# Kernel optimization log

Measured on AMD Instinct MI355X. Metric: run time of the kernel, lower is better.

Reference implementation:

```python
import jax, jax.numpy as jnp
import numpy as np


def _conv(x, w, b, stride, pad):
    y = jax.lax.conv_general_dilated(
        x, w, window_strides=(stride, stride),
        padding=((pad, pad), (pad, pad)),
        dimension_numbers=('NCHW', 'OIHW', 'NCHW'))
    return y + b[None, :, None, None]


def setup_inputs() -> dict:
    key = jax.random.key(0)
    ks = jax.random.split(key, 10)
    B, C, H, W = 4, 3, 256, 256
    HID, D, K = 128, 32, 65536
    s = 0.05
    return {
        'x': jax.random.normal(ks[0], (B, C, H, W), dtype=jnp.float32),
        'w1': jax.random.normal(ks[1], (HID, C, 4, 4), dtype=jnp.float32) * s,
        'b1': jnp.zeros((HID,), dtype=jnp.float32),
        'w2': jax.random.normal(ks[2], (HID, HID, 4, 4), dtype=jnp.float32) * s,
        'b2': jnp.zeros((HID,), dtype=jnp.float32),
        'w3': jax.random.normal(ks[3], (HID, HID, 4, 4), dtype=jnp.float32) * s,
        'b3': jnp.zeros((HID,), dtype=jnp.float32),
        'w4': jax.random.normal(ks[4], (D, HID, 3, 3), dtype=jnp.float32) * s,
        'b4': jnp.zeros((D,), dtype=jnp.float32),
        'codebook': jax.random.normal(ks[5], (K, D), dtype=jnp.float32),
    }


def reference(x, w1, b1, w2, b2, w3, b3, w4, b4, codebook):
    z = jax.nn.relu(_conv(x, w1, b1, 2, 1))
    z = jax.nn.relu(_conv(z, w2, b2, 2, 1))
    z = jax.nn.relu(_conv(z, w3, b3, 2, 1))
    z = _conv(z, w4, b4, 1, 1)                 # [B, D, h, w]
    z = jnp.transpose(z, (0, 2, 3, 1))          # [B, h, w, D]
    B, h, w, D = z.shape
    zf = z.reshape(-1, D)                        # [N, D]
    # pairwise squared distances: ||z||^2 + ||e||^2 - 2 z.e
    d = (jnp.sum(zf * zf, axis=1, keepdims=True)
         + jnp.sum(codebook * codebook, axis=1)[None, :]
         - 2.0 * jnp.matmul(zf, codebook.T))    # [N, K]
    idx = jnp.argmin(d, axis=1)                  # [N]
    z_q = codebook[idx].reshape(B, h, w, D)
    return idx.reshape(B, h, w), z_q
```

## Files before the change

### kernel.cpp

```cpp
#include <hip/hip_runtime.h>
#include <cfloat>

typedef float f32x4 __attribute__((ext_vector_type(4)));
typedef _Float16 h8 __attribute__((ext_vector_type(8)));

static __device__ __forceinline__ unsigned umin_(unsigned a, unsigned b) { return a < b ? a : b; }
static __device__ __forceinline__ unsigned umax_(unsigned a, unsigned b) { return a > b ? a : b; }
static __device__ __forceinline__ unsigned med3_(unsigned a, unsigned b, unsigned c) {
    unsigned d;
    asm("v_med3_u32 %0, %1, %2, %3" : "=v"(d) : "v"(a), "v"(b), "v"(c));
    return d;
}

static __device__ __forceinline__ void gl_lds16(const h8* g, h8* s) {
    __builtin_amdgcn_global_load_lds(
        (const __attribute__((address_space(1))) unsigned int*)g,
        (__attribute__((address_space(3))) unsigned int*)s, 16, 0, 0);
}


__global__ __launch_bounds__(256)
void zero_b_k(_Float16* p0, _Float16* p1, _Float16* p2, _Float16* p3,
              _Float16* p4, _Float16* p5) {
    const int s = blockIdx.y;
    _Float16* p; int np, P;
    switch (s) {
        case 0: p = p0; np = 16; P = 66; break;
        case 1: p = p1; np = 16; P = 66; break;
        case 2: p = p2; np = 16; P = 34; break;
        case 3: p = p3; np = 16; P = 34; break;
        case 4: p = p4; np = 4;  P = 34; break;
        default: p = p5; np = 4; P = 34; break;
    }
    const int plane = blockIdx.x;
    if (plane >= np) return;
    _Float16* pl = p + (size_t)plane * P * P * 128;
    const int rowN = P * 128;
    for (int i = threadIdx.x; i < rowN; i += 256) {
        pl[i] = (_Float16)0.f;
        pl[(size_t)(P - 1) * rowN + i] = (_Float16)0.f;
        const int r = i >> 7, c = i & 127;
        pl[(size_t)r * rowN + c] = (_Float16)0.f;
        pl[(size_t)r * rowN + (P - 1) * 128 + c] = (_Float16)0.f;
    }
}

__global__ __launch_bounds__(256)
void conv1_k(const float* __restrict__ in, const float* __restrict__ w,
             const float* __restrict__ bias,
             _Float16* __restrict__ Dh, _Float16* __restrict__ Dl) {
    __shared__ float tile[3][34 * 36];
    const int tid = threadIdx.x;
    const int tx = tid & 15, ty = tid >> 4;
    const int bx = blockIdx.x & 7, by = blockIdx.x >> 3;
    const int oc0 = blockIdx.y * 8;
    const int b = blockIdx.z;
    const int ox = bx * 16 + tx, oy = by * 16 + ty;
    const int ix0 = bx * 32 - 1, iy0 = by * 32 - 1;

    for (int f = tid; f < 3 * 34 * 34; f += 256) {
        const int ic = f / 1156, r2 = f % 1156;
        const int r = r2 / 34, c = r2 % 34;
        const int iy = iy0 + r, ix = ix0 + c;
        float v = ((unsigned)iy < 256u && (unsigned)ix < 256u)
                      ? in[((size_t)(b * 3 + ic) * 256 + iy) * 256 + ix] : 0.f;
        tile[ic][r * 36 + c] = v;
    }
    __syncthreads();

    float acc[8];
#pragma unroll
    for (int j = 0; j < 8; ++j) acc[j] = 0.f;
#pragma unroll
    for (int ic = 0; ic < 3; ++ic) {
#pragma unroll
        for (int kh = 0; kh < 4; ++kh) {
            const float2* p = (const float2*)&tile[ic][(2 * ty + kh) * 36 + 2 * tx];
            const float2 r0 = p[0], r1 = p[1];
            const float tap[4] = {r0.x, r0.y, r1.x, r1.y};
#pragma unroll
            for (int kw = 0; kw < 4; ++kw)
#pragma unroll
                for (int j = 0; j < 8; ++j)
                    acc[j] = fmaf(tap[kw], w[((oc0 + j) * 3 + ic) * 16 + kh * 4 + kw], acc[j]);
        }
    }

    h8 hv, lv;
#pragma unroll
    for (int j = 0; j < 8; ++j) {
        float r = fmaxf(acc[j] + bias[oc0 + j], 0.f);
        _Float16 h = (_Float16)r;
        hv[j] = h;
        lv[j] = (_Float16)((r - (float)h) * 2048.f);
    }
    const size_t di = (((size_t)((b * 2 + (oy & 1)) * 2 + (ox & 1)) * 66 + 1 + (oy >> 1)) * 66
                       + 1 + (ox >> 1)) * 128 + oc0;
    *(h8*)(Dh + di) = hv;
    *(h8*)(Dl + di) = lv;
}

__global__ __launch_bounds__(256)
void pack3_k(const float* __restrict__ w2, const float* __restrict__ w3,
             const float* __restrict__ w4,
             h8* __restrict__ B2h, h8* __restrict__ B2l,
             h8* __restrict__ B3h, h8* __restrict__ B3l,
             h8* __restrict__ B4h, h8* __restrict__ B4l) {
    const float* w; h8 *Bh, *Bl; int T, NT, KHKW;
    switch (blockIdx.y) {
        case 0:  w = w2; Bh = B2h; Bl = B2l; T = 16; NT = 8; KHKW = 16; break;
        case 1:  w = w3; Bh = B3h; Bl = B3l; T = 16; NT = 8; KHKW = 16; break;
        default: w = w4; Bh = B4h; Bl = B4l; T = 9;  NT = 2; KHKW = 9;  break;
    }
    const int idx = blockIdx.x * 256 + threadIdx.x;
    if (idx >= T * 4 * NT * 64) return;
    const int lane = idx & 63;
    int r = idx >> 6;
    const int nt = r % NT; r /= NT;
    const int ks = r & 3;  r >>= 2;
    const int t = r;
    const int oc = nt * 16 + (lane & 15);
    const int icb = ks * 32 + (lane >> 4) * 8;
    h8 hv, lv;
#pragma unroll
    for (int j = 0; j < 8; ++j) {
        const float v = w[(size_t)(oc * 128 + icb + j) * KHKW + t];
        _Float16 h = (_Float16)v;
        hv[j] = h;
        lv[j] = (_Float16)((v - (float)h) * 2048.f);
    }
    Bh[idx] = hv;
    Bl[idx] = lv;
}

template<int WN, int MT, bool SPLIT>
__global__ __launch_bounds__(256, 1)
void gemmS2_k(const _Float16* __restrict__ Ah, const _Float16* __restrict__ Al,
              const h8* __restrict__ Bh, const h8* __restrict__ Bl,
              const float* __restrict__ bias,
              _Float16* __restrict__ Dh, _Float16* __restrict__ Dl,
              int OW, int OH, int PP, int dPP) {
    constexpr int NW_N = 8 / WN;
    constexpr int NW_M = 4 / NW_N;
    __shared__ h8 lH[2][2048];
    __shared__ h8 lL[2][2048];

    const int tid = threadIdx.x, wid = tid >> 6, l = tid & 63;
    const int nq = wid % NW_N, mi = wid / NW_N;
    const int mt0 = (blockIdx.x * NW_M + mi) * MT;
    const int mpr = OW >> 4, mpi = OH * mpr;
    const int laneA = (l & 15) * 128 + (l >> 4) * 8;

    int bm[MT], oym[MT], oxm[MT];
#pragma unroll
    for (int m = 0; m < MT; ++m) {
        const int mt = mt0 + m;
        bm[m] = mt / mpi;
        const int rem = mt % mpi;
        oym[m] = rem / mpr;
        oxm[m] = (rem % mpr) << 4;
    }

    f32x4 a1[MT][WN], am[MT][WN];
#pragma unroll
    for (int m = 0; m < MT; ++m)
#pragma unroll
        for (int s = 0; s < WN; ++s) {
            a1[m][s] = (f32x4){0.f, 0.f, 0.f, 0.f};
            am[m][s] = (f32x4){0.f, 0.f, 0.f, 0.f};
        }

    {
        const h8* sh = Bh + wid * 512 + l;
        const h8* sl = Bl + wid * 512 + l;
#pragma unroll
        for (int i = 0; i < 8; ++i) gl_lds16(sh + i * 64, &lH[0][wid * 512 + i * 64]);
#pragma unroll
        for (int i = 0; i < 8; ++i) gl_lds16(sl + i * 64, &lL[0][wid * 512 + i * 64]);
    }
    __syncthreads();

#pragma unroll 1
    for (int t = 0; t < 16; ++t) {
        const int cur = t & 1;
        const int kh = t >> 2, kw = t & 3;
        const int dy = (kh - 1) >> 1, dx = (kw - 1) >> 1;
        const int py = (kh - 1) & 1, px = (kw - 1) & 1;
        h8 avh[MT][4], avl[MT][4];
#pragma unroll
        for (int m = 0; m < MT; ++m) {
            const int pidx = (bm[m] * 2 + py) * 2 + px;
            const size_t abase = ((size_t)(pidx * PP + (oym[m] + dy + 1)) * PP
                                  + (oxm[m] + dx + 1)) * 128 + laneA;
#pragma unroll
            for (int ks = 0; ks < 4; ++ks) {
                avh[m][ks] = *(const h8*)(Ah + abase + ks * 32);
                avl[m][ks] = *(const h8*)(Al + abase + ks * 32);
            }
        }
        if (t + 1 < 16) {
            const int nxt = cur ^ 1;
            const h8* sh = Bh + (size_t)(t + 1) * 2048 + wid * 512 + l;
            const h8* sl = Bl + (size_t)(t + 1) * 2048 + wid * 512 + l;
#pragma unroll
            for (int i = 0; i < 8; ++i) gl_lds16(sh + i * 64, &lH[nxt][wid * 512 + i * 64]);
#pragma unroll
            for (int i = 0; i < 8; ++i) gl_lds16(sl + i * 64, &lL[nxt][wid * 512 + i * 64]);
        }
#pragma unroll
        for (int ks = 0; ks < 4; ++ks) {
#pragma unroll
            for (int s = 0; s < WN; ++s) {
                const h8 bvh = lH[cur][(ks * 8 + nq * WN + s) * 64 + l];
                const h8 bvl = lL[cur][(ks * 8 + nq * WN + s) * 64 + l];
#pragma unroll
                for (int m = 0; m < MT; ++m) {
                    a1[m][s] = __builtin_amdgcn_mfma_f32_16x16x32_f16(avh[m][ks], bvh, a1[m][s], 0, 0, 0);
                    am[m][s] = __builtin_amdgcn_mfma_f32_16x16x32_f16(avh[m][ks], bvl, am[m][s], 0, 0, 0);
                    am[m][s] = __builtin_amdgcn_mfma_f32_16x16x32_f16(avl[m][ks], bvh, am[m][s], 0, 0, 0);
                }
            }
        }
        __syncthreads();
    }

#pragma unroll
    for (int m = 0; m < MT; ++m) {
#pragma unroll
        for (int s = 0; s < WN; ++s) {
            const int oc = (nq * WN + s) * 16 + (l & 15);
            const float bv = bias[oc];
#pragma unroll
            for (int i = 0; i < 4; ++i) {
                const int row = (l >> 4) * 4 + i;
                float v = fmaf(am[m][s][i], 4.8828125e-4f, a1[m][s][i]);
                v = fmaxf(v + bv, 0.f);
                _Float16 h = (_Float16)v;
                _Float16 lo = (_Float16)((v - (float)h) * 2048.f);
                const int oxp = oxm[m] + row;
                const int oy = oym[m], b = bm[m];
                size_t di;
                if constexpr (SPLIT) {
                    di = (((size_t)((b * 2 + (oy & 1)) * 2 + (oxp & 1)) * dPP
                           + 1 + (oy >> 1)) * dPP + 1 + (oxp >> 1)) * 128 + oc;
                } else {
                    di = ((size_t)(b * dPP + 1 + oy) * dPP + 1 + oxp) * 128 + oc;
                }
                Dh[di] = h;
                Dl[di] = lo;
            }
        }
    }
}

template<int S, bool FIN, int WPN, int MT>
__global__ __launch_bounds__(256)
void gemm_k(const _Float16* __restrict__ Ah, const _Float16* __restrict__ Al,
            const h8* __restrict__ Bh, const h8* __restrict__ Bl,
            float* __restrict__ part, const float* __restrict__ bias,
            _Float16* __restrict__ Dh, _Float16* __restrict__ Dl,
            int OW, int OH, int PP, int NT, int TPS, int M, int N, int dPP) {
    const int tid = threadIdx.x, wid = tid >> 6, l = tid & 63;
    const int ntb = wid % WPN;
    const int mt0 = (blockIdx.x * (4 / WPN) + wid / WPN) * MT;
    const int sp = blockIdx.y;
    const int mpr = OW >> 4, mpi = OH * mpr;
    const int laneA = (l & 15) * 128 + (l >> 4) * 8;

    int bmt[MT], oymt[MT], oxmt[MT];
#pragma unroll
    for (int m = 0; m < MT; ++m) {
        const int mt = mt0 + m;
        bmt[m] = mt / mpi;
        const int rem = mt % mpi;
        oymt[m] = rem / mpr;
        oxmt[m] = (rem % mpr) << 4;
    }

    f32x4 a1[MT][2], am[MT][2];
#pragma unroll
    for (int m = 0; m < MT; ++m)
#pragma unroll
        for (int s = 0; s < 2; ++s) {
            a1[m][s] = (f32x4){0.f, 0.f, 0.f, 0.f};
            am[m][s] = (f32x4){0.f, 0.f, 0.f, 0.f};
        }

    const int t0 = sp * TPS, t1 = t0 + TPS;
#pragma unroll 2
    for (int t = t0; t < t1; ++t) {
        int dy, dx, pidx[MT];
        if constexpr (S == 2) {
            const int kh = t >> 2, kw = t & 3;
            dy = (kh - 1) >> 1; dx = (kw - 1) >> 1;
            const int py = (kh - 1) & 1, px = (kw - 1) & 1;
#pragma unroll
            for (int m = 0; m < MT; ++m) pidx[m] = (bmt[m] * 2 + py) * 2 + px;
        } else {
            dy = t / 3 - 1; dx = t % 3 - 1;
#pragma unroll
            for (int m = 0; m < MT; ++m) pidx[m] = bmt[m];
        }
        const _Float16* pAh[MT]; const _Float16* pAl[MT];
#pragma unroll
        for (int m = 0; m < MT; ++m) {
            const size_t base = ((size_t)(pidx[m] * PP + (oymt[m] + dy + 1)) * PP
                                 + (oxmt[m] + dx + 1)) * 128 + laneA;
            pAh[m] = Ah + base;
            pAl[m] = Al + base;
        }
        const size_t bbase = ((size_t)(t * 4) * NT + ntb * 2) * 64 + l;
#pragma unroll
        for (int ks = 0; ks < 4; ++ks) {
            h8 avh[MT], avl[MT];
#pragma unroll
            for (int m = 0; m < MT; ++m) {
                avh[m] = *(const h8*)(pAh[m] + ks * 32);
                avl[m] = *(const h8*)(pAl[m] + ks * 32);
            }
#pragma unroll
            for (int s = 0; s < 2; ++s) {
                const h8 bvh = Bh[bbase + (size_t)ks * NT * 64 + s * 64];
                const h8 bvl = Bl[bbase + (size_t)ks * NT * 64 + s * 64];
#pragma unroll
                for (int m = 0; m < MT; ++m) {
                    a1[m][s] = __builtin_amdgcn_mfma_f32_16x16x32_f16(avh[m], bvh, a1[m][s], 0, 0, 0);
                    am[m][s] = __builtin_amdgcn_mfma_f32_16x16x32_f16(avh[m], bvl, am[m][s], 0, 0, 0);
                    am[m][s] = __builtin_amdgcn_mfma_f32_16x16x32_f16(avl[m], bvh, am[m][s], 0, 0, 0);
                }
            }
        }
    }

#pragma unroll
    for (int m = 0; m < MT; ++m) {
        const int mt = mt0 + m;
#pragma unroll
        for (int s = 0; s < 2; ++s) {
            const int oc = ntb * 32 + s * 16 + (l & 15);
#pragma unroll
            for (int i = 0; i < 4; ++i) {
                const int row = (l >> 4) * 4 + i;
                float v = fmaf(am[m][s][i], 4.8828125e-4f, a1[m][s][i]);
                if (!FIN) {
                    part[((size_t)sp * M + mt * 16 + row) * N + oc] = v;
                } else {
                    v = fmaxf(v + bias[oc], 0.f);
                    _Float16 h = (_Float16)v;
                    _Float16 lo = (_Float16)((v - (float)h) * 2048.f);
                    const int ox = oxmt[m] + row;
                    const int oy = oymt[m], b = bmt[m];
                    const size_t di = (((size_t)((b * 2 + (oy & 1)) * 2 + (ox & 1)) * dPP
                                        + 1 + (oy >> 1)) * dPP + 1 + (ox >> 1)) * 128 + oc;
                    Dh[di] = h;
                    Dl[di] = lo;
                }
            }
        }
    }
}

__global__ __launch_bounds__(256)
void fin4_k(const float* __restrict__ part, const float* __restrict__ bias,
            float* __restrict__ zz, h8* __restrict__ zh, h8* __restrict__ zl) {
    const int t = blockIdx.x * 256 + threadIdx.x;
    const int m = t >> 2, g8 = (t & 3) * 8;
    float v[8];
#pragma unroll
    for (int j = 0; j < 8; ++j) v[j] = bias[g8 + j];
#pragma unroll
    for (int sp = 0; sp < 3; ++sp) {
        const float4* p = (const float4*)(part + ((size_t)sp * 4096 + m) * 32 + g8);
        float4 x0 = p[0], x1 = p[1];
        v[0] += x0.x; v[1] += x0.y; v[2] += x0.z; v[3] += x0.w;
        v[4] += x1.x; v[5] += x1.y; v[6] += x1.z; v[7] += x1.w;
    }
    float4* dst = (float4*)(zz + (size_t)m * 32 + g8);
    dst[0] = make_float4(v[0], v[1], v[2], v[3]);
    dst[1] = make_float4(v[4], v[5], v[6], v[7]);
    h8 hv, lv;
#pragma unroll
    for (int j = 0; j < 8; ++j) {
        const float mv = -2.f * v[j];
        _Float16 h = (_Float16)mv;
        hv[j] = h;
        lv[j] = (_Float16)(mv - (float)h);
    }
    const int idx = (m >> 4) * 64 + (m & 15) + (t & 3) * 16;
    zh[idx] = hv;
    zl[idx] = lv;
}

#define VQ_NSPLIT 64
#define VQ_KSPC   1024
#define VQ_NCHUNK 8
#define VQ_TAU_S  102.4f
#define VQ_ABS_S  524288.0f
#define VQ_QT     4

__global__ __launch_bounds__(256)
void split_cb_k(const float* __restrict__ cb, h8* __restrict__ cbh, h8* __restrict__ cbl,
                float* __restrict__ cbn2, float* __restrict__ cbn_raw,
                unsigned* __restrict__ counter) {
    const int c = blockIdx.x * 256 + threadIdx.x;
    const float4* p = (const float4*)(cb + (size_t)c * 32);
    float e[32];
    float s = 0.f;
#pragma unroll
    for (int i = 0; i < 8; ++i) {
        float4 v = p[i];
        e[i*4+0] = v.x; e[i*4+1] = v.y; e[i*4+2] = v.z; e[i*4+3] = v.w;
        s += v.x*v.x + v.y*v.y + v.z*v.z + v.w*v.w;
    }
    cbn_raw[c] = s;
    cbn2[c]    = (s + 512.0f) * 2048.0f;
    const int base = (c >> 4) * 64 + (c & 15);
#pragma unroll
    for (int g = 0; g < 4; ++g) {
        h8 hv, lv;
#pragma unroll
        for (int j = 0; j < 8; ++j) {
            float v = e[g*8 + j];
            _Float16 h = (_Float16)v;
            hv[j] = (_Float16)((float)h * 2048.0f);
            lv[j] = (_Float16)((v - (float)h) * 2048.0f);
        }
        cbh[base + g*16] = hv;
        cbl[base + g*16] = lv;
    }
    if (c == 0) *counter = 0u;
}

__global__ __launch_bounds__(256, 4)
void vq_mfma_k(const h8* __restrict__ zh, const h8* __restrict__ zl,
               const uint4* __restrict__ cbh, const uint4* __restrict__ cbl,
               const float* __restrict__ cbn2,
               unsigned* __restrict__ pb1, unsigned* __restrict__ pb2,
               unsigned* __restrict__ pcol) {
    __shared__ uint4 lH[2][512];
    __shared__ uint4 lL[2][512];
    __shared__ float lN[2][128];

    const int tid = threadIdx.x;
    const int w = tid >> 6, ln = tid & 63;
    const int split = blockIdx.y;
    const int qt0 = (blockIdx.x * 4 + w) * VQ_QT;

    h8 azh[VQ_QT], azl[VQ_QT];
#pragma unroll
    for (int qq = 0; qq < VQ_QT; ++qq) {
        azh[qq] = zh[(qt0 + qq) * 64 + ln];
        azl[qq] = zl[(qt0 + qq) * 64 + ln];
    }

    unsigned b1[VQ_QT][4], b2[VQ_QT][4];
#pragma unroll
    for (int qq = 0; qq < VQ_QT; ++qq)
#pragma unroll
        for (int i = 0; i < 4; ++i) { b1[qq][i] = 0x7F800000u; b2[qq][i] = 0x7F800000u; }

    const int fbase = split * (VQ_KSPC * 4);
    const int nbase = split * VQ_KSPC;

    {
        uint4 h0 = cbh[fbase + tid], h1 = cbh[fbase + 256 + tid];
        uint4 l0 = cbl[fbase + tid], l1 = cbl[fbase + 256 + tid];
        lH[0][tid] = h0; lH[0][tid + 256] = h1;
        lL[0][tid] = l0; lL[0][tid + 256] = l1;
        if (tid < 128) lN[0][tid] = cbn2[nbase + tid];
    }
    __syncthreads();

    for (int ci = 0; ci < VQ_NCHUNK; ++ci) {
        const int cur = ci & 1;
        const bool more = (ci + 1 < VQ_NCHUNK);
        uint4 nh0, nh1, nl0, nl1; float nn = 0.f;
        if (more) {
            const int nb = fbase + (ci + 1) * 512;
            nh0 = cbh[nb + tid]; nh1 = cbh[nb + 256 + tid];
            nl0 = cbl[nb + tid]; nl1 = cbl[nb + 256 + tid];
            if (tid < 128) nn = cbn2[nbase + (ci + 1) * 128 + tid];
        }

        const unsigned tcb = (unsigned)(ci * 8);
#pragma unroll
        for (int t = 0; t < 8; ++t) {
            const h8 bh = *reinterpret_cast<const h8*>(&lH[cur][t*64 + ln]);
            const h8 bl = *reinterpret_cast<const h8*>(&lL[cur][t*64 + ln]);
            const float nv = lN[cur][t*16 + (ln & 15)];
            f32x4 nvv = {nv, nv, nv, nv};
            const unsigned tc = tcb + t;
#pragma unroll
            for (int qq = 0; qq < VQ_QT; ++qq) {
                f32x4 acc;
                acc = __builtin_amdgcn_mfma_f32_16x16x32_f16(azh[qq], bh, nvv, 0, 0, 0);
                acc = __builtin_amdgcn_mfma_f32_16x16x32_f16(azh[qq], bl, acc, 0, 0, 0);
                acc = __builtin_amdgcn_mfma_f32_16x16x32_f16(azl[qq], bh, acc, 0, 0, 0);
#pragma unroll
                for (int i = 0; i < 4; ++i) {
                    const unsigned k0 = (__float_as_uint(acc[i]) & 0xFFFFFF00u) | tc;
                    b2[qq][i] = med3_(b1[qq][i], b2[qq][i], k0);
                    b1[qq][i] = umin_(b1[qq][i], k0);
                }
            }
        }

        if (more) {
            const int nxt = cur ^ 1;
            lH[nxt][tid] = nh0; lH[nxt][tid + 256] = nh1;
            lL[nxt][tid] = nl0; lL[nxt][tid + 256] = nl1;
            if (tid < 128) lN[nxt][tid] = nn;
        }
        __syncthreads();
    }

#pragma unroll
    for (int qq = 0; qq < VQ_QT; ++qq) {
#pragma unroll
        for (int i = 0; i < 4; ++i) {
            unsigned v1 = b1[qq][i], v2 = b2[qq][i], cv = (unsigned)(ln & 15);
#pragma unroll
            for (int m = 1; m < 16; m <<= 1) {
                unsigned o1 = __shfl_xor(v1, m, 64);
                unsigned o2 = __shfl_xor(v2, m, 64);
                unsigned oc = __shfl_xor(cv, m, 64);
                unsigned nb2 = umin_(umin_(v2, o2), umax_(v1, o1));
                if (o1 < v1) cv = oc;
                v1 = umin_(v1, o1); v2 = nb2;
            }
            if ((ln & 15) == 0) {
                const int q = (qt0 + qq) * 16 + (ln >> 4) * 4 + i;
                pb1[(size_t)q * VQ_NSPLIT + split] = v1;
                pb2[(size_t)q * VQ_NSPLIT + split] = v2;
                pcol[(size_t)q * VQ_NSPLIT + split] = cv;
            }
        }
    }
}

__global__ __launch_bounds__(256)
void combine_k(const unsigned* __restrict__ pb1, const unsigned* __restrict__ pb2,
               const unsigned* __restrict__ pcol,
               unsigned* __restrict__ coarse, unsigned* __restrict__ flags,
               unsigned* __restrict__ list, unsigned* __restrict__ counter) {
    const int q = blockIdx.x * 256 + threadIdx.x;
    unsigned B1 = 0x7F800000u, B2 = 0x7F800000u, PAY = 0u;
#pragma unroll 4
    for (int s = 0; s < VQ_NSPLIT; ++s) {
        unsigned a1 = pb1[(size_t)q * VQ_NSPLIT + s];
        unsigned a2 = pb2[(size_t)q * VQ_NSPLIT + s];
        unsigned ac = pcol[(size_t)q * VQ_NSPLIT + s];
        unsigned nb2 = umin_(umin_(B2, a2), umax_(B1, a1));
        if (a1 < B1) PAY = ((unsigned)s << 4) | ac;
        B1 = umin_(B1, a1); B2 = nb2;
    }
    const unsigned tile = B1 & 0xFFu;
    const unsigned code = (PAY >> 4) * VQ_KSPC + tile * 16 + (PAY & 15u);
    const float f1 = __uint_as_float(B1 & 0xFFFFFF00u);
    const float f2 = __uint_as_float(B2 & 0xFFFFFF00u);
    const int fl = (f2 - f1 < VQ_TAU_S) || (f1 < VQ_ABS_S);
    coarse[q] = code;
    flags[q] = (unsigned)fl;
    if (fl) { unsigned p = atomicAdd(counter, 1u); list[p] = q; }
}

__global__ __launch_bounds__(256)
void guard_k(const float* __restrict__ cb, const float* __restrict__ cbn_raw,
             const float* __restrict__ zz, const unsigned* __restrict__ list,
             const unsigned* __restrict__ counter, float2* __restrict__ gpart) {
    __shared__ float lcb[256 * 36];
    __shared__ float lnr[256];
    __shared__ float2 red[4];
    __shared__ int ns;

    const int tid = threadIdx.x;
    const int w = tid >> 6, ln = tid & 63;
    const int bx = blockIdx.x;

    const float4* cb4 = (const float4*)cb;
#pragma unroll
    for (int it = 0; it < 8; ++it) {
        const int f = tid + it * 256;
        float4 v = cb4[(size_t)bx * 2048 + f];
        const int c = f >> 3, g = f & 7;
        *(float4*)&lcb[c * 36 + g * 4] = v;
    }
    lnr[tid] = cbn_raw[bx * 256 + tid];
    if (tid == 0) ns = (int)*(volatile unsigned*)counter;
    __syncthreads();

    for (int ii = blockIdx.y; ii < ns; ii += 8) {
        const int q = (int)list[ii];
        const float4* zq = (const float4*)(zz + (size_t)q * 32);
        float m2[32];
#pragma unroll
        for (int j = 0; j < 8; ++j) {
            float4 v = zq[j];
            m2[j*4+0] = -2.f*v.x; m2[j*4+1] = -2.f*v.y; m2[j*4+2] = -2.f*v.z; m2[j*4+3] = -2.f*v.w;
        }
        float d = lnr[tid];
#pragma unroll
        for (int j = 0; j < 8; ++j) {
            float4 e = *(const float4*)&lcb[tid * 36 + j * 4];
            d = fmaf(m2[j*4+0], e.x, d);
            d = fmaf(m2[j*4+1], e.y, d);
            d = fmaf(m2[j*4+2], e.z, d);
            d = fmaf(m2[j*4+3], e.w, d);
        }
        float bv = d; int bc = tid;
#pragma unroll
        for (int m = 1; m < 64; m <<= 1) {
            float ov = __shfl_xor(bv, m, 64);
            int   oi = __shfl_xor(bc, m, 64);
            if (ov < bv || (ov == bv && oi < bc)) { bv = ov; bc = oi; }
        }
        if (ln == 0) red[w] = make_float2(bv, (float)(bx * 256 + bc));
        __syncthreads();
        if (tid == 0) {
            float2 r = red[0];
#pragma unroll
            for (int k = 1; k < 4; ++k) {
                float2 o = red[k];
                if (o.x < r.x || (o.x == r.x && o.y < r.y)) r = o;
            }
            gpart[(size_t)q * 256 + bx] = r;
        }
        __syncthreads();
    }
}

__global__ __launch_bounds__(256)
void final_k(const unsigned* __restrict__ flags, const unsigned* __restrict__ coarse,
             const float2* __restrict__ gpart, const float* __restrict__ cb,
             float* __restrict__ out_idx, float* __restrict__ out_zq) {
    const int q = blockIdx.x * 256 + threadIdx.x;
    int bi;
    if (flags[q]) {
        float2 r = gpart[(size_t)q * 256];
        for (int b = 1; b < 256; ++b) {
            float2 o = gpart[(size_t)q * 256 + b];
            if (o.x < r.x || (o.x == r.x && o.y < r.y)) r = o;
        }
        bi = (int)r.y;
    } else {
        bi = (int)coarse[q];
    }
    out_idx[q] = (float)bi;
    const float4* src = (const float4*)(cb + (size_t)bi * 32);
    float4*       dst = (float4*)(out_zq + (size_t)q * 32);
#pragma unroll
    for (int i = 0; i < 8; ++i) dst[i] = src[i];
}

extern "C" void kernel_launch(void* const* d_in, const int* in_sizes, int n_in,
                              void* d_out, int out_size, void* d_ws, size_t ws_size,
                              hipStream_t stream) {
    const float* x  = (const float*)d_in[0];
    const float* w1 = (const float*)d_in[1];
    const float* b1 = (const float*)d_in[2];
    const float* w2 = (const float*)d_in[3];
    const float* b2 = (const float*)d_in[4];
    const float* w3 = (const float*)d_in[5];
    const float* b3 = (const float*)d_in[6];
    const float* w4 = (const float*)d_in[7];
    const float* b4 = (const float*)d_in[8];
    const float* cb = (const float*)d_in[9];
    float* out = (float*)d_out;

    float* ws = (float*)d_ws;
    _Float16* y1h = (_Float16*)ws;
    _Float16* y1l = (_Float16*)(ws + 4460544);
    _Float16* y2h = (_Float16*)(ws + 8921088);
    _Float16* y2l = (_Float16*)(ws + 10104832);
    _Float16* y3h = (_Float16*)(ws + 11288576);
    _Float16* y3l = (_Float16*)(ws + 11584512);
    float* zzp = ws + 11880448;
    h8* B2h = (h8*)(ws + 12011520);
    h8* B2l = (h8*)(ws + 12142592);
    h8* B3h = (h8*)(ws + 12273664);
    h8* B3l = (h8*)(ws + 12404736);
    h8* B4h = (h8*)(ws + 12535808);
    h8* B4l = (h8*)(ws + 12554240);
    float* part = ws + 12572672;
    h8*       cbh     = (h8*)ws;
    h8*       cbl     = (h8*)(ws + 1048576);
    h8*       zh      = (h8*)(ws + 2097152);
    h8*       zl      = (h8*)(ws + 2162688);
    float*    cbn2    = ws + 2228224;
    float*    cbn_raw = ws + 2293760;
    unsigned* pb1     = (unsigned*)(ws + 2359296);
    unsigned* pb2     = (unsigned*)(ws + 2621440);
    unsigned* pcol    = (unsigned*)(ws + 2883584);
    unsigned* coarse  = (unsigned*)(ws + 3145728);
    unsigned* flags   = (unsigned*)(ws + 3149824);
    unsigned* list    = (unsigned*)(ws + 3153920);
    unsigned* counter = (unsigned*)(ws + 3158016);
    float2*   gpart   = (float2*)(ws + 3158080);

    zero_b_k<<<dim3(16, 6), 256, 0, stream>>>(y1h, y1l, y2h, y2l, y3h, y3l);
    pack3_k<<<dim3(128, 3), 256, 0, stream>>>(w2, w3, w4, B2h, B2l, B3h, B3l, B4h, B4l);
    conv1_k<<<dim3(64, 16, 4), 256, 0, stream>>>(x, w1, b1, y1h, y1l);
    gemmS2_k<4, 2, true><<<dim3(256), 256, 0, stream>>>(y1h, y1l, B2h, B2l, b2, y2h, y2l,
                                                        64, 64, 66, 34);
    gemmS2_k<2, 1, false><<<dim3(256), 256, 0, stream>>>(y2h, y2l, B3h, B3l, b3, y3h, y3l,
                                                         32, 32, 34, 34);
    gemm_k<1, false, 1, 1><<<dim3(64, 3), 256, 0, stream>>>(y3h, y3l, B4h, B4l, part, nullptr, nullptr, nullptr,
                                                            32, 32, 34, 2, 3, 4096, 32, 0);
    fin4_k<<<64, 256, 0, stream>>>(part, b4, zzp, zh, zl);

    split_cb_k<<<256, 256, 0, stream>>>(cb, cbh, cbl, cbn2, cbn_raw, counter);
    vq_mfma_k <<<dim3(16, VQ_NSPLIT), 256, 0, stream>>>(zh, zl, (const uint4*)cbh, (const uint4*)cbl,
                                                        cbn2, pb1, pb2, pcol);
    combine_k <<<16,  256, 0, stream>>>(pb1, pb2, pcol, coarse, flags, list, counter);
    guard_k   <<<dim3(256, 8), 256, 0, stream>>>(cb, cbn_raw, zzp, list, counter, gpart);
    final_k   <<<16,  256, 0, stream>>>(flags, coarse, gpart, cb, out, out + 4096);
}
```

Measured before the change: 277.5 us.

## Give each wavefront its own query in guard and final reductions

In the guard kernel each wavefront now handles a separate flagged query and scans all 256 cached codes (4 per lane). This removes the block-wide LDS reduction and the two __syncthreads per query. The final kernel now assigns one wavefront per query and reduces the 256 partials with lanes plus shuffles, instead of one thread looping serially over 256 entries. It launches 1024 blocks instead of 16, which improves memory parallelism and spreads the gather copy across lanes.

```diff
diff --git a/kernel.cpp b/kernel.cpp
--- a/kernel.cpp
+++ b/kernel.cpp
@@ -570,7 +570,6 @@
              const unsigned* __restrict__ counter, float2* __restrict__ gpart) {
     __shared__ float lcb[256 * 36];
     __shared__ float lnr[256];
-    __shared__ float2 red[4];
     __shared__ int ns;
 
     const int tid = threadIdx.x;
@@ -589,7 +588,7 @@
     if (tid == 0) ns = (int)*(volatile unsigned*)counter;
     __syncthreads();
 
-    for (int ii = blockIdx.y; ii < ns; ii += 8) {
+    for (int ii = blockIdx.y * 4 + w; ii < ns; ii += 32) {
         const int q = (int)list[ii];
         const float4* zq = (const float4*)(zz + (size_t)q * 32);
         float m2[32];
@@ -598,34 +597,28 @@
             float4 v = zq[j];
             m2[j*4+0] = -2.f*v.x; m2[j*4+1] = -2.f*v.y; m2[j*4+2] = -2.f*v.z; m2[j*4+3] = -2.f*v.w;
         }
-        float d = lnr[tid];
-#pragma unroll
-        for (int j = 0; j < 8; ++j) {
-            float4 e = *(const float4*)&lcb[tid * 36 + j * 4];
-            d = fmaf(m2[j*4+0], e.x, d);
-            d = fmaf(m2[j*4+1], e.y, d);
-            d = fmaf(m2[j*4+2], e.z, d);
-            d = fmaf(m2[j*4+3], e.w, d);
-        }
-        float bv = d; int bc = tid;
+        float bv = FLT_MAX; int bc = 0x7FFFFFFF;
+#pragma unroll
+        for (int cc = 0; cc < 4; ++cc) {
+            const int c = cc * 64 + ln;
+            float d = lnr[c];
+#pragma unroll
+            for (int j = 0; j < 8; ++j) {
+                float4 e = *(const float4*)&lcb[c * 36 + j * 4];
+                d = fmaf(m2[j*4+0], e.x, d);
+                d = fmaf(m2[j*4+1], e.y, d);
+                d = fmaf(m2[j*4+2], e.z, d);
+                d = fmaf(m2[j*4+3], e.w, d);
+            }
+            if (d < bv || (d == bv && c < bc)) { bv = d; bc = c; }
+        }
 #pragma unroll
         for (int m = 1; m < 64; m <<= 1) {
             float ov = __shfl_xor(bv, m, 64);
             int   oi = __shfl_xor(bc, m, 64);
             if (ov < bv || (ov == bv && oi < bc)) { bv = ov; bc = oi; }
         }
-        if (ln == 0) red[w] = make_float2(bv, (float)(bx * 256 + bc));
-        __syncthreads();
-        if (tid == 0) {
-            float2 r = red[0];
-#pragma unroll
-            for (int k = 1; k < 4; ++k) {
-                float2 o = red[k];
-                if (o.x < r.x || (o.x == r.x && o.y < r.y)) r = o;
-            }
-            gpart[(size_t)q * 256 + bx] = r;
-        }
-        __syncthreads();
+        if (ln == 0) gpart[(size_t)q * 256 + bx] = make_float2(bv, (float)(bx * 256 + bc));
     }
 }
 
@@ -633,23 +626,33 @@
 void final_k(const unsigned* __restrict__ flags, const unsigned* __restrict__ coarse,
              const float2* __restrict__ gpart, const float* __restrict__ cb,
              float* __restrict__ out_idx, float* __restrict__ out_zq) {
-    const int q = blockIdx.x * 256 + threadIdx.x;
+    const int tid = threadIdx.x, w = tid >> 6, ln = tid & 63;
+    const int q = blockIdx.x * 4 + w;
     int bi;
     if (flags[q]) {
-        float2 r = gpart[(size_t)q * 256];
-        for (int b = 1; b < 256; ++b) {
+        float bv = FLT_MAX; int bidx = 0x7FFFFFFF;
+#pragma unroll
+        for (int k = 0; k < 4; ++k) {
+            const int b = k * 64 + ln;
             float2 o = gpart[(size_t)q * 256 + b];
-            if (o.x < r.x || (o.x == r.x && o.y < r.y)) r = o;
-        }
-        bi = (int)r.y;
+            int oi = (int)o.y;
+            if (o.x < bv || (o.x == bv && oi < bidx)) { bv = o.x; bidx = oi; }
+        }
+#pragma unroll
+        for (int m = 1; m < 64; m <<= 1) {
+            float ov = __shfl_xor(bv, m, 64);
+            int   oi = __shfl_xor(bidx, m, 64);
+            if (ov < bv || (ov == bv && oi < bidx)) { bv = ov; bidx = oi; }
+        }
+        bi = bidx;
     } else {
         bi = (int)coarse[q];
     }
-    out_idx[q] = (float)bi;
-    const float4* src = (const float4*)(cb + (size_t)bi * 32);
-    float4*       dst = (float4*)(out_zq + (size_t)q * 32);
-#pragma unroll
-    for (int i = 0; i < 8; ++i) dst[i] = src[i];
+    if (ln == 0) out_idx[q] = (float)bi;
+    if (ln < 8) {
+        float4 v = ((const float4*)(cb + (size_t)bi * 32))[ln];
+        ((float4*)(out_zq + (size_t)q * 32))[ln] = v;
+    }
 }
 
 extern "C" void kernel_launch(void* const* d_in, const int* in_sizes, int n_in,
@@ -713,5 +716,5 @@
                                                         cbn2, pb1, pb2, pcol);
     combine_k <<<16,  256, 0, stream>>>(pb1, pb2, pcol, coarse, flags, list, counter);
     guard_k   <<<dim3(256, 8), 256, 0, stream>>>(cb, cbn_raw, zzp, list, counter, gpart);
-    final_k   <<<16,  256, 0, stream>>>(flags, coarse, gpart, cb, out, out + 4096);
-}
+    final_k   <<<1024, 256, 0, stream>>>(flags, coarse, gpart, cb, out, out + 4096);
+}
```

Result: faster. 241.9 us (-12.8%).
